# Performance work log

Hardware: AMD Instinct MI355X
Metric: run time of the kernel (lower is better)

The kernel has to match this reference:

```python
import jax, jax.numpy as jnp
import numpy as np

B, N, HID, H, DH, NB = 4, 4096, 768, 12, 64, 266
EPS = 1e-4


def softmax_kernel(data, proj, is_query):
    # data: [B,H,N,DH], proj: [NB,DH]. FAVOR+ positive softmax features.
    d = data.shape[-1]
    ratio = proj.shape[0] ** -0.5
    dn = d ** -0.25  # data normalizer
    data_dash = jnp.einsum('bhnd,jd->bhnj', data * dn, proj)  # [B,H,N,NB]
    diag = 0.5 * jnp.sum((data * dn) ** 2, axis=-1, keepdims=True)  # [B,H,N,1]
    if is_query:
        m = jnp.max(data_dash, axis=-1, keepdims=True)
    else:
        m = jnp.max(data_dash, axis=(-1, -2), keepdims=True)
    return ratio * (jnp.exp(data_dash - diag - m) + EPS)


def setup_inputs() -> dict:
    key = jax.random.key(0)
    ks = jax.random.split(key, 8)
    s = HID ** -0.5
    return {
        'hidden_states': jax.random.normal(ks[0], (B, N, HID), jnp.float32),
        'Wq': jax.random.normal(ks[1], (HID, HID), jnp.float32) * s,
        'bq': jnp.zeros((HID,), jnp.float32),
        'Wk': jax.random.normal(ks[2], (HID, HID), jnp.float32) * s,
        'bk': jnp.zeros((HID,), jnp.float32),
        'Wv': jax.random.normal(ks[3], (HID, HID), jnp.float32) * s,
        'bv': jnp.zeros((HID,), jnp.float32),
        'proj': jax.random.normal(ks[4], (NB, DH), jnp.float32),
    }


def reference(hidden_states, Wq, bq, Wk, bk, Wv, bv, proj):
    def heads(x):  # [B,N,HID] -> [B,H,N,DH]
        return x.reshape(B, N, H, DH).transpose(0, 2, 1, 3)

    q = heads(hidden_states @ Wq.T + bq)
    k = heads(hidden_states @ Wk.T + bk)
    v = heads(hidden_states @ Wv.T + bv)

    qp = softmax_kernel(q, proj, True)   # [B,H,N,NB]
    kp = softmax_kernel(k, proj, False)  # [B,H,N,NB]

    # non-causal linear attention: out = q' (k'^T v) / (q' sum_n k')
    k_sum = jnp.sum(kp, axis=2)                               # [B,H,NB]
    d_inv = 1.0 / jnp.einsum('bhnj,bhj->bhn', qp, k_sum)      # [B,H,N]
    ctx = jnp.einsum('bhnj,bhnd->bhjd', kp, v)                # [B,H,NB,DH]
    out = jnp.einsum('bhnj,bhjd->bhnd', qp, ctx) * d_inv[..., None]

    return out.transpose(0, 2, 1, 3).reshape(B, N, HID)
```

## Files before the change

### kernel.cpp

```cpp
#include <hip/hip_runtime.h>
#include <hip/hip_bf16.h>
#include <stdint.h>

#define B_   4
#define N_   4096
#define HID_ 768
#define H_   12
#define DH_  64
#define NB_  266
#define NBP_ 288
#define EPS_ 1e-4f
#define RATIO_ 0.06131393f

typedef unsigned short u16;
typedef __attribute__((ext_vector_type(8))) short short8;
typedef __attribute__((ext_vector_type(4))) float floatx4;

__device__ __forceinline__ u16 f2b(float f) {
  __hip_bfloat16 h = __float2bfloat16(f);
  return *reinterpret_cast<u16*>(&h);
}
__device__ __forceinline__ float b2f(u16 u) {
  union { unsigned u; float f; } x; x.u = ((unsigned)u) << 16; return x.f;
}
__device__ __forceinline__ unsigned fmap(float x) {
  unsigned u = __float_as_uint(x);
  return (u & 0x80000000u) ? ~u : (u | 0x80000000u);
}
__device__ __forceinline__ float funmap(unsigned u) {
  unsigned b = (u & 0x80000000u) ? (u & 0x7FFFFFFFu) : ~u;
  return __uint_as_float(b);
}
__device__ __forceinline__ void gl16(const u16* g, u16* l) {
  __builtin_amdgcn_global_load_lds(
      (const __attribute__((address_space(1))) void*)g,
      (__attribute__((address_space(3))) void*)l, 16, 0, 0);
}

__global__ __launch_bounds__(256) void k_prep(
    const float4* __restrict__ hs, const float4* __restrict__ Wq,
    const float4* __restrict__ Wk, const float4* __restrict__ Wv,
    const float* __restrict__ proj,
    uint2* __restrict__ hsb, uint2* __restrict__ wb3, u16* __restrict__ projb,
    unsigned* __restrict__ mbuf) {
  int blk = blockIdx.x;
  const int t = threadIdx.x;
  if (blk < 12288) {
    int i = blk * 256 + t;
    float4 v = hs[i];
    union { u16 s[4]; uint2 u; } pk;
    pk.s[0] = f2b(v.x); pk.s[1] = f2b(v.y); pk.s[2] = f2b(v.z); pk.s[3] = f2b(v.w);
    hsb[i] = pk.u;
    return;
  }
  blk -= 12288;
  if (blk < 1728) {
    int i = blk * 256 + t;
    int sel = i / 147456, j = i - sel * 147456;
    const float4* s = (sel == 0) ? Wq : (sel == 1) ? Wk : Wv;
    float4 v = s[j];
    union { u16 s4[4]; uint2 u; } pk;
    pk.s4[0] = f2b(v.x); pk.s4[1] = f2b(v.y); pk.s4[2] = f2b(v.z); pk.s4[3] = f2b(v.w);
    wb3[i] = pk.u;
    return;
  }
  blk -= 1728;
  if (blk < 72) {
    int i = blk * 256 + t;
    int j = i / DH_, d = i - j * DH_;
    float v = (j < NB_) ? proj[j * DH_ + d] * 0.35355339059327373f : 0.f;
    projb[i] = f2b(v);
    return;
  }
  blk -= 72;
  if (blk == 0 && t < B_ * H_) mbuf[t] = 0u;
}

__global__ __launch_bounds__(256) void k_qkv(
    const u16* __restrict__ hsb, const u16* __restrict__ wb,
    const float* __restrict__ bq, const float* __restrict__ bk, const float* __restrict__ bv,
    u16* __restrict__ qb, u16* __restrict__ kb, u16* __restrict__ vT) {
  __shared__ u16 At[2 * 128 * 32];
  __shared__ u16 Bt[2 * 128 * 32];
  const int m0 = blockIdx.x * 128;
  const int bn = blockIdx.y;
  const int sel = bn / 6;
  const int or0 = (bn % 6) * 128;
  const u16* W = wb + (size_t)sel * HID_ * HID_;
  const int t = threadIdx.x, lane = t & 63, wv = t >> 6;
  const int wr = (wv >> 1) * 64, wc = (wv & 1) * 64;
  const int lm = lane & 15, lq = lane >> 4;
  const int srow = wv * 32 + (lane >> 2);
  const int scol = (lane & 3) * 8;
  const u16* gA = hsb + (size_t)(m0 + srow) * HID_ + scol;
  const u16* gB = W + (size_t)(or0 + srow) * HID_ + scol;
  u16* lA = At + wv * 1024;
  u16* lB = Bt + wv * 1024;
  floatx4 acc[4][4];
#pragma unroll
  for (int i = 0; i < 4; i++)
#pragma unroll
    for (int j = 0; j < 4; j++) acc[i][j] = (floatx4){0.f, 0.f, 0.f, 0.f};

  for (int k0 = 0; k0 < HID_; k0 += 64) {
    __syncthreads();
#pragma unroll
    for (int p = 0; p < 2; p++) {
#pragma unroll
      for (int i = 0; i < 2; i++) {
        gl16(gA + k0 + p * 32 + i * 16 * HID_, lA + p * 4096 + i * 512);
        gl16(gB + k0 + p * 32 + i * 16 * HID_, lB + p * 4096 + i * 512);
      }
    }
    __syncthreads();
#pragma unroll
    for (int p = 0; p < 2; p++) {
      short8 af[4], bfr[4];
#pragma unroll
      for (int mt = 0; mt < 4; mt++) af[mt] = *(const short8*)&At[p * 4096 + (wr + mt * 16 + lm) * 32 + lq * 8];
#pragma unroll
      for (int nt = 0; nt < 4; nt++) bfr[nt] = *(const short8*)&Bt[p * 4096 + (wc + nt * 16 + lm) * 32 + lq * 8];
#pragma unroll
      for (int mt = 0; mt < 4; mt++)
#pragma unroll
        for (int nt = 0; nt < 4; nt++)
          acc[mt][nt] = __builtin_amdgcn_mfma_f32_16x16x32_bf16(af[mt], bfr[nt], acc[mt][nt], 0, 0, 0);
    }
  }
  if (sel < 2) {
    const float* bias = (sel == 0) ? bq : bk;
    u16* dst = (sel == 0) ? qb : kb;
#pragma unroll
    for (int mt = 0; mt < 4; mt++) {
#pragma unroll
      for (int nt = 0; nt < 4; nt++) {
        int lc = or0 + wc + nt * 16 + lm;
        float bb = bias[lc];
#pragma unroll
        for (int r = 0; r < 4; r++) {
          int row = m0 + wr + mt * 16 + lq * 4 + r;
          dst[(size_t)row * HID_ + lc] = f2b(acc[mt][nt][r] + bb);
        }
      }
    }
  } else {
#pragma unroll
    for (int mt = 0; mt < 4; mt++) {
#pragma unroll
      for (int nt = 0; nt < 4; nt++) {
        int lc = or0 + wc + nt * 16 + lm;
        int hh = lc >> 6, dv = lc & 63;
        float bb = bv[lc];
        int rowbase = m0 + wr + mt * 16 + lq * 4;
        int b = rowbase >> 12, n = rowbase & 4095;
        union { u16 s[4]; uint2 u; } pk;
#pragma unroll
        for (int r = 0; r < 4; r++) pk.s[r] = f2b(acc[mt][nt][r] + bb);
        *(uint2*)(vT + ((size_t)(b * H_ + hh) * DH_ + dv) * N_ + n) = pk.u;
      }
    }
  }
}

__global__ __launch_bounds__(256) void k_kmax3(
    const u16* __restrict__ kb, const u16* __restrict__ projb,
    unsigned* __restrict__ mbuf, float* __restrict__ diagk) {
  const int bh = blockIdx.y, b = bh / H_, h = bh - b * H_;
  const int n0 = blockIdx.x * 256;
  const int t = threadIdx.x, lane = t & 63, wv = t >> 6;
  const int lm = lane & 15, lq = lane >> 4;
  const u16* kbase = kb + (size_t)(b * N_ + n0 + wv * 64) * HID_ + h * DH_;
  short8 af0[4], af1[4];
#pragma unroll
  for (int mt = 0; mt < 4; mt++) {
    const u16* p = kbase + (size_t)(mt * 16 + lm) * HID_ + lq * 8;
    af0[mt] = *(const short8*)p;
    af1[mt] = *(const short8*)(p + 32);
  }
#pragma unroll
  for (int mt = 0; mt < 4; mt++) {
    float rs = 0.f;
#pragma unroll
    for (int i = 0; i < 8; i++) { float f = b2f(((const u16*)&af0[mt])[i]); rs += f * f; }
#pragma unroll
    for (int i = 0; i < 8; i++) { float f = b2f(((const u16*)&af1[mt])[i]); rs += f * f; }
    rs += __shfl_xor(rs, 16);
    rs += __shfl_xor(rs, 32);
    if (lq == 0) diagk[(size_t)bh * N_ + n0 + wv * 64 + mt * 16 + lm] = 0.0625f * rs;
  }
  float mx = -3e38f;
  for (int ct = 0; ct < 17; ct++) {
    const u16* pp = projb + (ct * 16 + lm) * DH_ + lq * 8;
    short8 bf0 = *(const short8*)pp;
    short8 bf1 = *(const short8*)(pp + 32);
    bool valid = (ct < 16) || (lm < 10);
#pragma unroll
    for (int mt = 0; mt < 4; mt++) {
      floatx4 a = __builtin_amdgcn_mfma_f32_16x16x32_bf16(af0[mt], bf0, (floatx4){0.f,0.f,0.f,0.f}, 0, 0, 0);
      a = __builtin_amdgcn_mfma_f32_16x16x32_bf16(af1[mt], bf1, a, 0, 0, 0);
      if (valid) {
#pragma unroll
        for (int r = 0; r < 4; r++) mx = fmaxf(mx, a[r]);
      }
    }
  }
#pragma unroll
  for (int o = 1; o < 64; o <<= 1) mx = fmaxf(mx, __shfl_xor(mx, o));
  if (lane == 0) atomicMax(&mbuf[bh], fmap(mx));
}

__global__ __launch_bounds__(256) void k_ctx4(
    const u16* __restrict__ kb, const u16* __restrict__ vT, const u16* __restrict__ projb,
    const unsigned* __restrict__ mbuf, const float* __restrict__ diagk,
    float* __restrict__ ksum, u16* __restrict__ ctxb) {
  __shared__ u16 kpl[32 * 72];
  __shared__ float kred[4][2][16];
  const int orig = blockIdx.x;
  const int lg = (orig & 7) * 54 + (orig >> 3);
  const int bh = lg / 9, jb = lg - bh * 9;
  const int j0 = jb * 32;
  const int b = bh / H_, h = bh - b * H_;
  const int t = threadIdx.x, lane = t & 63, wv = t >> 6;
  const int lm = lane & 15, lq = lane >> 4;
  const float m = funmap(mbuf[bh]);
  const bool vj0 = (j0 + lm) < NB_;
  const bool vj1 = (j0 + 16 + lm) < NB_;
  short8 bp00, bp01, bp10, bp11;
  {
    const u16* pp = projb + (j0 + lm) * DH_ + lq * 8;
    bp00 = *(const short8*)pp;
    bp01 = *(const short8*)(pp + 32);
    pp += 16 * DH_;
    bp10 = *(const short8*)pp;
    bp11 = *(const short8*)(pp + 32);
  }
  const u16* kbB = kb + (size_t)(b * N_) * HID_ + h * DH_;
  const u16* vTb = vT + ((size_t)bh * DH_ + wv * 16 + lm) * N_;
  const float* dgB = diagk + (size_t)bh * N_;
  floatx4 acc0 = (floatx4){0.f,0.f,0.f,0.f}, acc1 = (floatx4){0.f,0.f,0.f,0.f};
  float kacc0 = 0.f, kacc1 = 0.f;
  const u16* kr0 = kbB + (size_t)(wv * 16 + lm) * HID_ + lq * 8;
  short8 af0 = *(const short8*)kr0;
  short8 af1 = *(const short8*)(kr0 + 32);
  floatx4 dg4 = *(const floatx4*)(dgB + wv * 16 + lq * 4);

  for (int n64 = 0; n64 < N_; n64 += 64) {
    __syncthreads();
    const int nn = (n64 + 64 < N_) ? n64 + 64 : 0;
    const u16* krn = kbB + (size_t)(nn + wv * 16 + lm) * HID_ + lq * 8;
    short8 nf0 = *(const short8*)krn;
    short8 nf1 = *(const short8*)(krn + 32);
    floatx4 nd = *(const floatx4*)(dgB + nn + wv * 16 + lq * 4);
    short8 av0 = *(const short8*)(vTb + n64 + lq * 8);
    short8 av1 = *(const short8*)(vTb + n64 + 32 + lq * 8);
    {
      floatx4 a = __builtin_amdgcn_mfma_f32_16x16x32_bf16(af0, bp00, (floatx4){0.f,0.f,0.f,0.f}, 0, 0, 0);
      a = __builtin_amdgcn_mfma_f32_16x16x32_bf16(af1, bp01, a, 0, 0, 0);
      union { u16 s[4]; uint2 u; } pk;
      float kss = 0.f;
#pragma unroll
      for (int r = 0; r < 4; r++) {
        float val = vj0 ? RATIO_ * (__expf(a[r] - dg4[r] - m) + EPS_) : 0.f;
        kss += val;
        pk.s[r] = f2b(val);
      }
      kacc0 += kss;
      *(uint2*)&kpl[lm * 72 + wv * 16 + lq * 4] = pk.u;
      a = __builtin_amdgcn_mfma_f32_16x16x32_bf16(af0, bp10, (floatx4){0.f,0.f,0.f,0.f}, 0, 0, 0);
      a = __builtin_amdgcn_mfma_f32_16x16x32_bf16(af1, bp11, a, 0, 0, 0);
      kss = 0.f;
#pragma unroll
      for (int r = 0; r < 4; r++) {
        float val = vj1 ? RATIO_ * (__expf(a[r] - dg4[r] - m) + EPS_) : 0.f;
        kss += val;
        pk.s[r] = f2b(val);
      }
      kacc1 += kss;
      *(uint2*)&kpl[(16 + lm) * 72 + wv * 16 + lq * 4] = pk.u;
    }
    __syncthreads();
    {
      short8 bf = *(const short8*)&kpl[lm * 72 + lq * 8];
      acc0 = __builtin_amdgcn_mfma_f32_16x16x32_bf16(av0, bf, acc0, 0, 0, 0);
      bf = *(const short8*)&kpl[(16 + lm) * 72 + lq * 8];
      acc1 = __builtin_amdgcn_mfma_f32_16x16x32_bf16(av0, bf, acc1, 0, 0, 0);
      bf = *(const short8*)&kpl[lm * 72 + 32 + lq * 8];
      acc0 = __builtin_amdgcn_mfma_f32_16x16x32_bf16(av1, bf, acc0, 0, 0, 0);
      bf = *(const short8*)&kpl[(16 + lm) * 72 + 32 + lq * 8];
      acc1 = __builtin_amdgcn_mfma_f32_16x16x32_bf16(av1, bf, acc1, 0, 0, 0);
    }
    af0 = nf0; af1 = nf1; dg4 = nd;
  }
  {
    float v0 = kacc0; v0 += __shfl_xor(v0, 16); v0 += __shfl_xor(v0, 32);
    float v1 = kacc1; v1 += __shfl_xor(v1, 16); v1 += __shfl_xor(v1, 32);
    if (lq == 0) { kred[wv][0][lm] = v0; kred[wv][1][lm] = v1; }
  }
  __syncthreads();
  if (t < 32) {
    int jh = t >> 4, l = t & 15;
    ksum[bh * NBP_ + j0 + t] =
        kred[0][jh][l] + kred[1][jh][l] + kred[2][jh][l] + kred[3][jh][l];
  }
  {
    u16* cb = ctxb + ((size_t)bh * DH_ + wv * 16 + lq * 4) * NBP_ + j0 + lm;
#pragma unroll
    for (int r = 0; r < 4; r++) {
      cb[(size_t)r * NBP_] = f2b(acc0[r]);
      cb[(size_t)r * NBP_ + 16] = f2b(acc1[r]);
    }
  }
}

__global__ __launch_bounds__(256) void k_out3(
    const u16* __restrict__ qb, const u16* __restrict__ projb,
    const u16* __restrict__ ctxb, const float* __restrict__ ksum,
    float* __restrict__ outp) {
  __shared__ u16 qpl[4][16][296];
  const int bh = blockIdx.y, b = bh / H_, h = bh - b * H_;
  const int n0 = blockIdx.x * 256;
  const int t = threadIdx.x, lane = t & 63, wv = t >> 6;
  const int lm = lane & 15, lq = lane >> 4;
  const u16* qbase = qb + (size_t)(b * N_ + n0 + wv * 64) * HID_ + h * DH_;
  const u16* cb = ctxb + (size_t)bh * DH_ * NBP_;
  const float* ksb = ksum + bh * NBP_;
  float ksv[17];
#pragma unroll
  for (int ct = 0; ct < 17; ct++) ksv[ct] = ksb[ct * 16 + lm];

  for (int mt = 0; mt < 4; mt++) {
    const u16* prow = qbase + (size_t)(mt * 16 + lm) * HID_ + lq * 8;
    short8 af0 = *(const short8*)prow;
    short8 af1 = *(const short8*)(prow + 32);
    float rs = 0.f;
#pragma unroll
    for (int i = 0; i < 8; i++) { float f = b2f(((const u16*)&af0)[i]); rs += f * f; }
#pragma unroll
    for (int i = 0; i < 8; i++) { float f = b2f(((const u16*)&af1)[i]); rs += f * f; }
    rs += __shfl_xor(rs, 16);
    rs += __shfl_xor(rs, 32);
    float dg[4];
#pragma unroll
    for (int r = 0; r < 4; r++) dg[r] = 0.0625f * __shfl(rs, lq * 4 + r);

    float rm[4] = {-3e38f, -3e38f, -3e38f, -3e38f};
#pragma unroll
    for (int ct = 0; ct < 17; ct++) {
      const u16* pp = projb + (ct * 16 + lm) * DH_ + lq * 8;
      short8 bf0 = *(const short8*)pp;
      short8 bf1 = *(const short8*)(pp + 32);
      floatx4 a = __builtin_amdgcn_mfma_f32_16x16x32_bf16(af0, bf0, (floatx4){0.f,0.f,0.f,0.f}, 0, 0, 0);
      a = __builtin_amdgcn_mfma_f32_16x16x32_bf16(af1, bf1, a, 0, 0, 0);
      if ((ct < 16) || (lm < 10)) {
#pragma unroll
        for (int r = 0; r < 4; r++) rm[r] = fmaxf(rm[r], a[r]);
      }
    }
#pragma unroll
    for (int o = 1; o < 16; o <<= 1) {
#pragma unroll
      for (int r = 0; r < 4; r++) rm[r] = fmaxf(rm[r], __shfl_xor(rm[r], o));
    }
    float dpart[4] = {0.f, 0.f, 0.f, 0.f};
#pragma unroll
    for (int ct = 0; ct < 18; ct++) {
      floatx4 a;
      if (ct < 17) {
        const u16* pp = projb + (ct * 16 + lm) * DH_ + lq * 8;
        short8 bf0 = *(const short8*)pp;
        short8 bf1 = *(const short8*)(pp + 32);
        a = __builtin_amdgcn_mfma_f32_16x16x32_bf16(af0, bf0, (floatx4){0.f,0.f,0.f,0.f}, 0, 0, 0);
        a = __builtin_amdgcn_mfma_f32_16x16x32_bf16(af1, bf1, a, 0, 0, 0);
      } else {
        a = (floatx4){0.f, 0.f, 0.f, 0.f};
      }
      bool valid = (ct < 16) || (ct == 16 && lm < 10);
      float kv = (ct < 17) ? ksv[ct] : 0.f;
#pragma unroll
      for (int r = 0; r < 4; r++) {
        float qpv = valid ? RATIO_ * (__expf(a[r] - dg[r] - rm[r]) + EPS_) : 0.f;
        dpart[r] += qpv * kv;
        qpl[wv][lq * 4 + r][ct * 16 + lm] = f2b(qpv);
      }
    }
#pragma unroll
    for (int o = 1; o < 16; o <<= 1) {
#pragma unroll
      for (int r = 0; r < 4; r++) dpart[r] += __shfl_xor(dpart[r], o);
    }
    float dinv[4];
#pragma unroll
    for (int r = 0; r < 4; r++) dinv[r] = 1.f / dpart[r];

    floatx4 ao[4];
#pragma unroll
    for (int dt = 0; dt < 4; dt++) ao[dt] = (floatx4){0.f, 0.f, 0.f, 0.f};
#pragma unroll
    for (int ks9 = 0; ks9 < 9; ks9++) {
      short8 aq = *(const short8*)&qpl[wv][lm][ks9 * 32 + lq * 8];
#pragma unroll
      for (int dt = 0; dt < 4; dt++) {
        short8 bc = *(const short8*)(cb + (size_t)(dt * 16 + lm) * NBP_ + ks9 * 32 + lq * 8);
        ao[dt] = __builtin_amdgcn_mfma_f32_16x16x32_bf16(aq, bc, ao[dt], 0, 0, 0);
      }
    }
#pragma unroll
    for (int dt = 0; dt < 4; dt++) {
#pragma unroll
      for (int r = 0; r < 4; r++) {
        int n = n0 + wv * 64 + mt * 16 + lq * 4 + r;
        outp[((size_t)(b * N_ + n)) * HID_ + h * DH_ + dt * 16 + lm] = ao[dt][r] * dinv[r];
      }
    }
  }
}

extern "C" void kernel_launch(void* const* d_in, const int* in_sizes, int n_in,
                              void* d_out, int out_size, void* d_ws, size_t ws_size,
                              hipStream_t stream) {
  (void)in_sizes; (void)n_in; (void)out_size; (void)ws_size;
  const float* hs   = (const float*)d_in[0];
  const float* Wq   = (const float*)d_in[1];
  const float* bq   = (const float*)d_in[2];
  const float* Wk   = (const float*)d_in[3];
  const float* bk   = (const float*)d_in[4];
  const float* Wv   = (const float*)d_in[5];
  const float* bv   = (const float*)d_in[6];
  const float* proj = (const float*)d_in[7];

  char* w = (char*)d_ws;
  u16* hsb   = (u16*)w;  w += (size_t)16384 * 768 * 2;
  u16* wb3   = (u16*)w;  w += (size_t)3 * 768 * 768 * 2;
  u16* projb = (u16*)w;  w += (size_t)NBP_ * 64 * 2;
  u16* qb    = (u16*)w;  w += (size_t)16384 * 768 * 2;
  u16* kb    = (u16*)w;  w += (size_t)16384 * 768 * 2;
  u16* vT    = (u16*)w;  w += (size_t)48 * DH_ * N_ * 2;
  float* ksum  = (float*)w; w += (size_t)48 * NBP_ * 4;
  float* diagk = (float*)w; w += (size_t)48 * N_ * 4;
  u16* ctxTb = (u16*)w;  w += (size_t)48 * DH_ * NBP_ * 2;
  unsigned* mbuf = (unsigned*)w;

  hipLaunchKernelGGL(k_prep, dim3(14089), dim3(256), 0, stream,
                     (const float4*)hs, (const float4*)Wq, (const float4*)Wk, (const float4*)Wv,
                     proj, (uint2*)hsb, (uint2*)wb3, projb, mbuf);
  hipLaunchKernelGGL(k_qkv, dim3(128, 18), dim3(256), 0, stream, hsb, wb3, bq, bk, bv, qb, kb, vT);
  hipLaunchKernelGGL(k_kmax3, dim3(16, 48), dim3(256), 0, stream, kb, projb, mbuf, diagk);
  hipLaunchKernelGGL(k_ctx4, dim3(432), dim3(256), 0, stream, kb, vT, projb, mbuf, diagk, ksum, ctxTb);
  hipLaunchKernelGGL(k_out3, dim3(16, 48), dim3(256), 0, stream, qb, projb, ctxTb, ksum, (float*)d_out);
}
```

Measured before the change: 365.9 us.

## Rewrite QKV GEMM with 256x256 tiles, triple-buffered LDS, swizzle and XCD remap

Replaces the QKV projection GEMM with a 512-thread kernel computing 256x256 output tiles. It uses a three-stage LDS ring fed by direct global-to-LDS loads and overlaps the next loads with MFMA work using vmcnt waits and one barrier per k-step. It also XOR-swizzles LDS columns to cut bank conflicts and remaps block IDs so neighbouring tiles land on the same XCD. The aim is to raise arithmetic intensity and hide memory latency, at the cost of more registers and LDS per block, which lowers occupancy.

Measured after the change: 364.4 us. About the same (-0.4%).

```diff
diff --git a/kernel.cpp b/kernel.cpp
--- a/kernel.cpp
+++ b/kernel.cpp
@@ -76,82 +76,97 @@
   if (blk == 0 && t < B_ * H_) mbuf[t] = 0u;
 }
 
-__global__ __launch_bounds__(256) void k_qkv(
+__global__ __launch_bounds__(512, 2) void k_qkv2(
     const u16* __restrict__ hsb, const u16* __restrict__ wb,
     const float* __restrict__ bq, const float* __restrict__ bk, const float* __restrict__ bv,
     u16* __restrict__ qb, u16* __restrict__ kb, u16* __restrict__ vT) {
-  __shared__ u16 At[2 * 128 * 32];
-  __shared__ u16 Bt[2 * 128 * 32];
-  const int m0 = blockIdx.x * 128;
-  const int bn = blockIdx.y;
-  const int sel = bn / 6;
-  const int or0 = (bn % 6) * 128;
+  __shared__ u16 lds[3 * 16384];
+  const int orig = blockIdx.x;
+  const int lg = (orig & 7) * 72 + (orig >> 3);
+  const int tm = lg / 9, tn = lg - tm * 9;
+  const int m0 = tm * 256;
+  const int c0 = tn * 256;
+  const int sel = c0 / 768;
+  const int or0 = c0 - sel * 768;
   const u16* W = wb + (size_t)sel * HID_ * HID_;
   const int t = threadIdx.x, lane = t & 63, wv = t >> 6;
-  const int wr = (wv >> 1) * 64, wc = (wv & 1) * 64;
   const int lm = lane & 15, lq = lane >> 4;
-  const int srow = wv * 32 + (lane >> 2);
-  const int scol = (lane & 3) * 8;
-  const u16* gA = hsb + (size_t)(m0 + srow) * HID_ + scol;
-  const u16* gB = W + (size_t)(or0 + srow) * HID_ + scol;
-  u16* lA = At + wv * 1024;
-  u16* lB = Bt + wv * 1024;
-  floatx4 acc[4][4];
-#pragma unroll
-  for (int i = 0; i < 4; i++)
-#pragma unroll
-    for (int j = 0; j < 4; j++) acc[i][j] = (floatx4){0.f, 0.f, 0.f, 0.f};
-
-  for (int k0 = 0; k0 < HID_; k0 += 64) {
-    __syncthreads();
-#pragma unroll
-    for (int p = 0; p < 2; p++) {
-#pragma unroll
-      for (int i = 0; i < 2; i++) {
-        gl16(gA + k0 + p * 32 + i * 16 * HID_, lA + p * 4096 + i * 512);
-        gl16(gB + k0 + p * 32 + i * 16 * HID_, lB + p * 4096 + i * 512);
-      }
-    }
-    __syncthreads();
-#pragma unroll
-    for (int p = 0; p < 2; p++) {
-      short8 af[4], bfr[4];
-#pragma unroll
-      for (int mt = 0; mt < 4; mt++) af[mt] = *(const short8*)&At[p * 4096 + (wr + mt * 16 + lm) * 32 + lq * 8];
-#pragma unroll
-      for (int nt = 0; nt < 4; nt++) bfr[nt] = *(const short8*)&Bt[p * 4096 + (wc + nt * 16 + lm) * 32 + lq * 8];
-#pragma unroll
-      for (int mt = 0; mt < 4; mt++)
-#pragma unroll
-        for (int nt = 0; nt < 4; nt++)
-          acc[mt][nt] = __builtin_amdgcn_mfma_f32_16x16x32_bf16(af[mt], bfr[nt], acc[mt][nt], 0, 0, 0);
-    }
-  }
+  const int wvm = wv >> 2, wvn = wv & 3;
+  const int srow = t >> 2;
+  const int scol = ((t & 3) ^ ((t >> 3) & 3)) * 8;
+  const u16* gA0 = hsb + (size_t)(m0 + srow) * HID_ + scol;
+  const u16* gB0 = W + (size_t)(or0 + srow) * HID_ + scol;
+  u16* lb = lds + wv * 512;
+  const int slotc = (lq ^ ((lm >> 1) & 3)) * 8;
+  const int aoff = (wvm * 128 + lm) * 32 + slotc;
+  const int boff = 8192 + (wvn * 64 + lm) * 32 + slotc;
+
+  floatx4 acc[8][4];
+#pragma unroll
+  for (int mt = 0; mt < 8; mt++)
+#pragma unroll
+    for (int nt = 0; nt < 4; nt++) acc[mt][nt] = (floatx4){0.f, 0.f, 0.f, 0.f};
+
+#define STAGE_QKV(kt)                                            \
+  {                                                              \
+    const int k0_ = (kt) * 32;                                   \
+    u16* l_ = lb + ((kt) % 3) * 16384;                           \
+    gl16(gA0 + k0_, l_);                                         \
+    gl16(gA0 + 128 * HID_ + k0_, l_ + 4096);                     \
+    gl16(gB0 + k0_, l_ + 8192);                                  \
+    gl16(gB0 + 128 * HID_ + k0_, l_ + 12288);                    \
+  }
+
+  STAGE_QKV(0);
+  STAGE_QKV(1);
+  asm volatile("s_waitcnt vmcnt(4)" ::: "memory");
+  __builtin_amdgcn_s_barrier();
+
+  for (int kt = 0; kt < 24; ++kt) {
+    if (kt + 2 < 24) STAGE_QKV(kt + 2);
+    const u16* bufA = lds + (kt % 3) * 16384;
+    short8 af[8], bf[4];
+#pragma unroll
+    for (int mt = 0; mt < 8; mt++) af[mt] = *(const short8*)&bufA[aoff + mt * 512];
+#pragma unroll
+    for (int nt = 0; nt < 4; nt++) bf[nt] = *(const short8*)&bufA[boff + nt * 512];
+    __builtin_amdgcn_s_setprio(1);
+#pragma unroll
+    for (int mt = 0; mt < 8; mt++)
+#pragma unroll
+      for (int nt = 0; nt < 4; nt++)
+        acc[mt][nt] = __builtin_amdgcn_mfma_f32_16x16x32_bf16(af[mt], bf[nt], acc[mt][nt], 0, 0, 0);
+    __builtin_amdgcn_s_setprio(0);
+    if (kt < 22) asm volatile("s_waitcnt vmcnt(4)" ::: "memory");
+    else         asm volatile("s_waitcnt vmcnt(0)" ::: "memory");
+    __builtin_amdgcn_s_barrier();
+  }
+#undef STAGE_QKV
+
   if (sel < 2) {
     const float* bias = (sel == 0) ? bq : bk;
     u16* dst = (sel == 0) ? qb : kb;
 #pragma unroll
-    for (int mt = 0; mt < 4; mt++) {
-#pragma unroll
-      for (int nt = 0; nt < 4; nt++) {
-        int lc = or0 + wc + nt * 16 + lm;
-        float bb = bias[lc];
-#pragma unroll
-        for (int r = 0; r < 4; r++) {
-          int row = m0 + wr + mt * 16 + lq * 4 + r;
-          dst[(size_t)row * HID_ + lc] = f2b(acc[mt][nt][r] + bb);
-        }
+    for (int nt = 0; nt < 4; nt++) {
+      int lc = or0 + wvn * 64 + nt * 16 + lm;
+      float bb = bias[lc];
+#pragma unroll
+      for (int mt = 0; mt < 8; mt++) {
+        int rowb = m0 + wvm * 128 + mt * 16 + lq * 4;
+#pragma unroll
+        for (int r = 0; r < 4; r++)
+          dst[(size_t)(rowb + r) * HID_ + lc] = f2b(acc[mt][nt][r] + bb);
       }
     }
   } else {
 #pragma unroll
-    for (int mt = 0; mt < 4; mt++) {
-#pragma unroll
-      for (int nt = 0; nt < 4; nt++) {
-        int lc = or0 + wc + nt * 16 + lm;
-        int hh = lc >> 6, dv = lc & 63;
-        float bb = bv[lc];
-        int rowbase = m0 + wr + mt * 16 + lq * 4;
+    for (int nt = 0; nt < 4; nt++) {
+      int lc = or0 + wvn * 64 + nt * 16 + lm;
+      int hh = lc >> 6, dv = lc & 63;
+      float bb = bv[lc];
+#pragma unroll
+      for (int mt = 0; mt < 8; mt++) {
+        int rowbase = m0 + wvm * 128 + mt * 16 + lq * 4;
         int b = rowbase >> 12, n = rowbase & 4095;
         union { u16 s[4]; uint2 u; } pk;
 #pragma unroll
@@ -443,7 +458,7 @@
   hipLaunchKernelGGL(k_prep, dim3(14089), dim3(256), 0, stream,
                      (const float4*)hs, (const float4*)Wq, (const float4*)Wk, (const float4*)Wv,
                      proj, (uint2*)hsb, (uint2*)wb3, projb, mbuf);
-  hipLaunchKernelGGL(k_qkv, dim3(128, 18), dim3(256), 0, stream, hsb, wb3, bq, bk, bv, qb, kb, vT);
+  hipLaunchKernelGGL(k_qkv2, dim3(576), dim3(512), 0, stream, hsb, wb3, bq, bk, bv, qb, kb, vT);
   hipLaunchKernelGGL(k_kmax3, dim3(16, 48), dim3(256), 0, stream, kb, projb, mbuf, diagk);
   hipLaunchKernelGGL(k_ctx4, dim3(432), dim3(256), 0, stream, kb, vT, projb, mbuf, diagk, ksum, ctxTb);
   hipLaunchKernelGGL(k_out3, dim3(16, 48), dim3(256), 0, stream, qb, projb, ctxTb, ksum, (float*)d_out);
```
